# Kernel tuning notes

Hardware: AMD Instinct MI355X
Metric: run time of the kernel (lower is better)

The kernel has to match this reference:

```python
import jax, jax.numpy as jnp
import numpy as np

B, S, H = 32, 256, 256
D = 2 * H          # BiLSTM output dim (hidden_dim*2)
F = 1024           # total fragment count across the batch
T = 5              # tagset size


def setup_inputs() -> dict:
    key = jax.random.key(0)
    ks = jax.random.split(key, 9)
    en_output = jax.random.normal(ks[0], (B, S, D), jnp.float32)
    # descending lengths, first sentence defines seq_length = S
    lengths = jnp.sort(jax.random.randint(ks[1], (B,), S // 2, S + 1))[::-1]
    lengths = lengths.at[0].set(S)
    frag_b = jax.random.randint(ks[2], (F,), 0, B)
    frag_s = jax.random.randint(ks[3], (F,), 0, S // 2 - 8)
    width = jax.random.randint(ks[4], (F,), 1, 8)
    frag_e = frag_s + width  # end exclusive, always <= lengths[frag_b]
    att_w = jax.random.normal(ks[5], (3 * D, D), jnp.float32) / np.float32(np.sqrt(3 * D))
    att_b = jax.random.normal(ks[6], (3 * D,), jnp.float32) * 0.01
    tag_w = jax.random.normal(ks[7], (T, 4 * D), jnp.float32) / np.float32(np.sqrt(4 * D))
    tag_b = jax.random.normal(ks[8], (T,), jnp.float32) * 0.01
    return {"en_output": en_output, "lengths": lengths, "frag_b": frag_b,
            "frag_s": frag_s, "frag_e": frag_e, "att_w": att_w, "att_b": att_b,
            "tag_w": tag_w, "tag_b": tag_b}


def reference(en_output, lengths, frag_b, frag_s, frag_e, att_w, att_b, tag_w, tag_b):
    Fn = frag_b.shape[0]
    Bn, Sn, Dn = en_output.shape
    dtype = en_output.dtype
    pos = jnp.arange(Sn)                                            # [S]
    in_span = (pos[None, :] >= frag_s[:, None]) & (pos[None, :] < frag_e[:, None])  # [F,S]
    memory = en_output[frag_b]                                      # [F,S,D] gather per fragment
    # word_state = sum of hidden states over the span (segment-sum via mask)
    word_state = jnp.einsum('fs,fsd->fd', in_span.astype(dtype), memory)
    l_word = en_output[frag_b, frag_s]                              # [F,D]
    r_word = en_output[frag_b, frag_e - 1]                          # [F,D]
    span = jnp.concatenate([l_word, word_state, r_word], axis=-1)   # [F,3D]
    # attention mask: the span itself and all padding positions are masked out
    att_mask = in_span | (pos[None, :] >= lengths[frag_b][:, None])  # [F,S]
    seq_len = lengths[0]
    # position distance (int), then position weight 1 - dist/seq_len
    pos_dis = jnp.where(pos[None, :] < frag_s[:, None], frag_s[:, None] - pos[None, :],
                jnp.where(pos[None, :] >= frag_e[:, None], pos[None, :] - frag_e[:, None] + 1,
                          seq_len)).astype(dtype)
    pos_weight = 1.0 - pos_dis / seq_len.astype(dtype)
    final = pos_weight[:, :, None] * memory                         # [F,S,D]
    # att(final) @ span == final @ (att_w.T span) + att_b.span ; att_w is [3D, D] (torch Linear weight)
    v = span @ att_w                                                # [F,D]
    c = span @ att_b                                                # [F]
    scores = jnp.tanh(jnp.einsum('fsd,fd->fs', final, v) + c[:, None])
    scores = jnp.where(att_mask, jnp.asarray(-1e4, dtype), scores)
    att = jax.nn.softmax(scores, axis=1)                            # [F,S]
    mix = jnp.einsum('fs,fsd->fd', att, final)                      # [F,D]
    mix_state = jnp.concatenate([span, mix], axis=-1)               # [F,4D]
    logits = mix_state @ tag_w.T + tag_b                            # [F,T]
    return jax.nn.log_softmax(logits, axis=1)
```

## Files before the change

### kernel.cpp

```cpp
#include <hip/hip_runtime.h>
#include <math.h>

#define BB 32
#define SS 256
#define DD 512
#define FF 1024
#define TT 5
#define K3 1536
#define K4 2048
#define GK 1536
#define SK 4
#define KCH (GK / SK)

__device__ __forceinline__ float wave_reduce_sum(float x) {
#pragma unroll
  for (int o = 32; o > 0; o >>= 1) x += __shfl_xor(x, o);
  return x;
}

__device__ __forceinline__ float row16_sum(float x) {
  int y;
  y = __builtin_amdgcn_mov_dpp(__float_as_int(x), 0x121, 0xf, 0xf, true);
  x += __int_as_float(y);
  y = __builtin_amdgcn_mov_dpp(__float_as_int(x), 0x122, 0xf, 0xf, true);
  x += __int_as_float(y);
  y = __builtin_amdgcn_mov_dpp(__float_as_int(x), 0x124, 0xf, 0xf, true);
  x += __int_as_float(y);
  y = __builtin_amdgcn_mov_dpp(__float_as_int(x), 0x128, 0xf, 0xf, true);
  x += __int_as_float(y);
  return x;
}

__device__ __forceinline__ float fast_tanh(float x) {
  float ax = fabsf(x);
  float t = __expf(-2.f * ax);
  float r = (1.f - t) / (1.f + t);
  return x < 0.f ? -r : r;
}

__global__ __launch_bounds__(1024)
void bucket_kernel(const int* __restrict__ fb, int* __restrict__ order) {
  __shared__ int cnt[BB];
  __shared__ int start[BB];
  int t = threadIdx.x;
  if (t < BB) cnt[t] = 0;
  __syncthreads();
  int b = fb[t];
  int r = atomicAdd(&cnt[b], 1);
  __syncthreads();
  if (t == 0) {
    int pos = 0;
    for (int x = 0; x < 8; ++x) {
      int sb[4] = {x, 15 - x, 16 + x, 31 - x};
      for (int j = 0; j < 4; ++j) { start[sb[j]] = pos; pos += cnt[sb[j]]; }
    }
  }
  __syncthreads();
  order[start[b] + r] = t;
}

__global__ __launch_bounds__(128)
void span_kernel(const float* __restrict__ en, const int* __restrict__ fb,
                 const int* __restrict__ fs, const int* __restrict__ fe,
                 const float* __restrict__ att_b, const int* __restrict__ order,
                 float* __restrict__ span, float* __restrict__ cvec)
{
  int bid = blockIdx.x;
  int f = order[(bid & 7) * (FF / 8) + (bid >> 3)];
  int t = threadIdx.x;
  int b = fb[f], s = fs[f], e = fe[f];
  const float* base = en + (size_t)b * SS * DD;
  int d0 = t * 4;
  float4 lw = *(const float4*)(base + (size_t)s * DD + d0);
  float4 rw = *(const float4*)(base + (size_t)(e - 1) * DD + d0);
  float4 wsum = make_float4(0.f, 0.f, 0.f, 0.f);
  for (int p = s; p < e; ++p) {
    float4 m = *(const float4*)(base + (size_t)p * DD + d0);
    wsum.x += m.x; wsum.y += m.y; wsum.z += m.z; wsum.w += m.w;
  }
  float* sp = span + (size_t)f * K3;
  *(float4*)(sp + d0) = lw;
  *(float4*)(sp + DD + d0) = wsum;
  *(float4*)(sp + 2 * DD + d0) = rw;
  float4 a0 = *(const float4*)(att_b + d0);
  float4 a1 = *(const float4*)(att_b + DD + d0);
  float4 a2 = *(const float4*)(att_b + 2 * DD + d0);
  float part = lw.x*a0.x + lw.y*a0.y + lw.z*a0.z + lw.w*a0.w
             + wsum.x*a1.x + wsum.y*a1.y + wsum.z*a1.z + wsum.w*a1.w
             + rw.x*a2.x + rw.y*a2.y + rw.z*a2.z + rw.w*a2.w;
  part = wave_reduce_sum(part);
  __shared__ float red[2];
  if ((t & 63) == 0) red[t >> 6] = part;
  __syncthreads();
  if (t == 0) cvec[f] = red[0] + red[1];
}

__global__ __launch_bounds__(256)
void gemm_v(const float* __restrict__ A,
            const float* __restrict__ Bw,
            float* __restrict__ Cpart)
{
  const int BM = 64, BN = 64, BK = 16;
  const int NIT = KCH / BK;
  __shared__ float As[BK][BM + 4];
  __shared__ float Bs[BK][BN + 4];
  int t = threadIdx.x;
  int n0 = blockIdx.x * BN;
  int m0 = blockIdx.y * BM;
  int kbase = blockIdx.z * KCH;

  int ar = t >> 2;
  int ac = (t & 3) * 4;
  int br = t >> 4;
  int bc = (t & 15) * 4;
  int tm = (t >> 4) * 4;
  int tn = (t & 15) * 4;

  float acc[4][4] = {};

  const float* Aptr = A  + (size_t)(m0 + ar) * GK + kbase + ac;
  const float* Bptr = Bw + (size_t)(kbase + br) * DD + n0 + bc;

  float4 av = *(const float4*)(Aptr);
  float4 bv = *(const float4*)(Bptr);

  for (int it = 0; it < NIT; ++it) {
    __syncthreads();
    As[ac + 0][ar] = av.x;
    As[ac + 1][ar] = av.y;
    As[ac + 2][ar] = av.z;
    As[ac + 3][ar] = av.w;
    *(float4*)(&Bs[br][bc]) = bv;
    __syncthreads();
    if (it + 1 < NIT) {
      av = *(const float4*)(Aptr + (it + 1) * BK);
      bv = *(const float4*)(Bptr + (size_t)(it + 1) * BK * DD);
    }
#pragma unroll
    for (int k = 0; k < BK; ++k) {
      float4 a = *(float4*)(&As[k][tm]);
      float4 b = *(float4*)(&Bs[k][tn]);
      acc[0][0] += a.x * b.x; acc[0][1] += a.x * b.y; acc[0][2] += a.x * b.z; acc[0][3] += a.x * b.w;
      acc[1][0] += a.y * b.x; acc[1][1] += a.y * b.y; acc[1][2] += a.y * b.z; acc[1][3] += a.y * b.w;
      acc[2][0] += a.z * b.x; acc[2][1] += a.z * b.y; acc[2][2] += a.z * b.z; acc[2][3] += a.z * b.w;
      acc[3][0] += a.w * b.x; acc[3][1] += a.w * b.y; acc[3][2] += a.w * b.z; acc[3][3] += a.w * b.w;
    }
  }
  float* Cp = Cpart + (size_t)blockIdx.z * FF * DD;
#pragma unroll
  for (int i = 0; i < 4; ++i) {
    *(float4*)(Cp + (size_t)(m0 + tm + i) * DD + n0 + tn) =
        make_float4(acc[i][0], acc[i][1], acc[i][2], acc[i][3]);
  }
}

__global__ __launch_bounds__(256, 4)
void frag_kernel(const float* __restrict__ en, const int* __restrict__ lengths,
                 const int* __restrict__ fb, const int* __restrict__ fs,
                 const int* __restrict__ fe,
                 const float* __restrict__ span, const float* __restrict__ cvec,
                 const float* __restrict__ vpart,
                 const float* __restrict__ tag_w, const float* __restrict__ tag_b,
                 const int* __restrict__ order,
                 float* __restrict__ out)
{
  __shared__ float v_lds[DD];
  __shared__ float buf[4][DD];
  __shared__ float wsum[4];
  __shared__ float mix_lds[DD];
  __shared__ float pl[4 * TT];
  __shared__ float l5[TT];

  int bid = blockIdx.x;
  int f = order[(bid & 7) * (FF / 8) + (bid >> 3)];
  int t = threadIdx.x;
  int lane = t & 63, wv = t >> 6;
  int b = fb[f], s = fs[f], e = fe[f];
  int lenb = lengths[b];
  float seqlen = (float)lengths[0];
  float invseq = 1.f / seqlen;
  float c = cvec[f];
  const float* mem = en + (size_t)b * SS * DD;

  if (t < 128) {
    float4 v0 = *(const float4*)(vpart + (size_t)f * DD + t * 4);
    float4 v1 = *(const float4*)(vpart + (size_t)FF * DD + (size_t)f * DD + t * 4);
    float4 v2 = *(const float4*)(vpart + 2 * (size_t)FF * DD + (size_t)f * DD + t * 4);
    float4 v3 = *(const float4*)(vpart + 3 * (size_t)FF * DD + (size_t)f * DD + t * 4);
    *(float4*)(v_lds + t * 4) = make_float4(v0.x + v1.x + v2.x + v3.x,
                                            v0.y + v1.y + v2.y + v3.y,
                                            v0.z + v1.z + v2.z + v3.z,
                                            v0.w + v1.w + v2.w + v3.w);
  }
  __syncthreads();

  float4 va = *(float4*)(v_lds + lane * 8);
  float4 vb = *(float4*)(v_lds + lane * 8 + 4);
  float ssum = 0.f;
  float am[8] = {0.f, 0.f, 0.f, 0.f, 0.f, 0.f, 0.f, 0.f};

  int rows = lenb - wv * 64;
  if (rows > 64) rows = 64;
  for (int i0 = 0; i0 < rows; i0 += 8) {
    float4 R0[8], R1[8];
    float d8[8];
#pragma unroll
    for (int k = 0; k < 8; ++k) {
      if (i0 + k < rows) {
        int p = wv * 64 + i0 + k;
        const float* row = mem + (size_t)p * DD + lane * 8;
        R0[k] = *(const float4*)(row);
        R1[k] = *(const float4*)(row + 4);
        d8[k] = R0[k].x*va.x + R0[k].y*va.y + R0[k].z*va.z + R0[k].w*va.w
              + R1[k].x*vb.x + R1[k].y*vb.y + R1[k].z*vb.z + R1[k].w*vb.w;
      } else {
        d8[k] = 0.f;
      }
    }
#pragma unroll
    for (int k = 0; k < 8; ++k) d8[k] = row16_sum(d8[k]);
#pragma unroll
    for (int k = 0; k < 8; ++k) d8[k] += __shfl_xor(d8[k], 16);
#pragma unroll
    for (int k = 0; k < 8; ++k) d8[k] += __shfl_xor(d8[k], 32);
#pragma unroll
    for (int k = 0; k < 8; ++k) {
      int p = wv * 64 + i0 + k;
      bool live = (i0 + k < rows) && !(p >= s && p < e);
      if (live) {
        float dis = (p < s) ? (float)(s - p) : (float)(p - e + 1);
        float pw = 1.f - dis * invseq;
        float sc = fast_tanh(pw * d8[k] + c);
        float u = __expf(sc - 1.f);
        ssum += u;
        float upw = u * pw;
        am[0] += upw * R0[k].x; am[1] += upw * R0[k].y; am[2] += upw * R0[k].z; am[3] += upw * R0[k].w;
        am[4] += upw * R1[k].x; am[5] += upw * R1[k].y; am[6] += upw * R1[k].z; am[7] += upw * R1[k].w;
      }
    }
  }
  if (lane == 0) wsum[wv] = ssum;
  *(float4*)(&buf[wv][lane * 8])     = make_float4(am[0], am[1], am[2], am[3]);
  *(float4*)(&buf[wv][lane * 8 + 4]) = make_float4(am[4], am[5], am[6], am[7]);
  __syncthreads();
  {
    float S = wsum[0] + wsum[1] + wsum[2] + wsum[3];
    float inv = 1.f / S;
    int d0 = t * 2;
    mix_lds[d0]     = (buf[0][d0] + buf[1][d0] + buf[2][d0] + buf[3][d0]) * inv;
    mix_lds[d0 + 1] = (buf[0][d0 + 1] + buf[1][d0 + 1] + buf[2][d0 + 1] + buf[3][d0 + 1]) * inv;
  }
  __syncthreads();

  float vals[8];
  int idx = t * 8;
  if (idx < K3) {
    const float* sp = span + (size_t)f * K3 + idx;
    float4 x0 = *(const float4*)(sp);
    float4 x1 = *(const float4*)(sp + 4);
    vals[0]=x0.x; vals[1]=x0.y; vals[2]=x0.z; vals[3]=x0.w;
    vals[4]=x1.x; vals[5]=x1.y; vals[6]=x1.z; vals[7]=x1.w;
  } else {
#pragma unroll
    for (int j = 0; j < 8; ++j) vals[j] = mix_lds[idx - K3 + j];
  }
  float acc5[TT];
#pragma unroll
  for (int tg = 0; tg < TT; ++tg) {
    const float* twr = tag_w + (size_t)tg * K4 + idx;
    float a = 0.f;
#pragma unroll
    for (int j = 0; j < 8; ++j) a += vals[j] * twr[j];
    acc5[tg] = wave_reduce_sum(a);
  }
  if (lane == 0) {
#pragma unroll
    for (int tg = 0; tg < TT; ++tg) pl[wv * TT + tg] = acc5[tg];
  }
  __syncthreads();
  if (t < TT) {
    l5[t] = pl[t] + pl[TT + t] + pl[2 * TT + t] + pl[3 * TT + t] + tag_b[t];
  }
  __syncthreads();
  if (t == 0) {
    float mm = l5[0];
#pragma unroll
    for (int j = 1; j < TT; ++j) mm = fmaxf(mm, l5[j]);
    float se = 0.f;
#pragma unroll
    for (int j = 0; j < TT; ++j) se += __expf(l5[j] - mm);
    float lse = mm + logf(se);
#pragma unroll
    for (int j = 0; j < TT; ++j) out[(size_t)f * TT + j] = l5[j] - lse;
  }
}

extern "C" void kernel_launch(void* const* d_in, const int* in_sizes, int n_in,
                              void* d_out, int out_size, void* d_ws, size_t ws_size,
                              hipStream_t stream) {
  const float* en      = (const float*)d_in[0];
  const int*   lengths = (const int*)d_in[1];
  const int*   frag_b  = (const int*)d_in[2];
  const int*   frag_s  = (const int*)d_in[3];
  const int*   frag_e  = (const int*)d_in[4];
  const float* att_w   = (const float*)d_in[5];
  const float* att_b   = (const float*)d_in[6];
  const float* tag_w   = (const float*)d_in[7];
  const float* tag_b   = (const float*)d_in[8];
  float* out = (float*)d_out;

  float* span  = (float*)d_ws;
  float* cvec  = span + (size_t)FF * K3;
  float* vpart = cvec + FF;
  int*   order = (int*)(vpart + (size_t)SK * FF * DD);

  bucket_kernel<<<1, FF, 0, stream>>>(frag_b, order);
  span_kernel<<<FF, 128, 0, stream>>>(en, frag_b, frag_s, frag_e, att_b, order, span, cvec);
  gemm_v<<<dim3(8, 16, SK), 256, 0, stream>>>(span, att_w, vpart);
  frag_kernel<<<FF, 256, 0, stream>>>(en, lengths, frag_b, frag_s, frag_e,
                                      span, cvec, vpart, tag_w, tag_b, order, out);
}
```

Baseline: 146.0 us.

## Split each wave into four 16-lane groups processing separate rows

Restructures the attention scan so each wave processes four sequence rows at once, each handled by a 16-lane group covering the full 512-wide row. This removes the cross-row shuffle reductions (xor 16/32) per row, leaving only a DPP row16 reduction. In exchange, per-thread accumulators grow to 32 floats plus 32 staged values, and the partial-sum LDS buffer grows fourfold to 16 partials, raising register and LDS pressure.

Result: faster. 130.9 us (-10.3%).

```diff
diff --git a/kernel.cpp b/kernel.cpp
--- a/kernel.cpp
+++ b/kernel.cpp
@@ -165,8 +165,8 @@
                  float* __restrict__ out)
 {
   __shared__ float v_lds[DD];
-  __shared__ float buf[4][DD];
-  __shared__ float wsum[4];
+  __shared__ float buf[16][DD];
+  __shared__ float wsum[16];
   __shared__ float mix_lds[DD];
   __shared__ float pl[4 * TT];
   __shared__ float l5[TT];
@@ -175,6 +175,8 @@
   int f = order[(bid & 7) * (FF / 8) + (bid >> 3)];
   int t = threadIdx.x;
   int lane = t & 63, wv = t >> 6;
+  int g = lane >> 4;
+  int j = lane & 15;
   int b = fb[f], s = fs[f], e = fe[f];
   int lenb = lengths[b];
   float seqlen = (float)lengths[0];
@@ -194,61 +196,65 @@
   }
   __syncthreads();
 
-  float4 va = *(float4*)(v_lds + lane * 8);
-  float4 vb = *(float4*)(v_lds + lane * 8 + 4);
+  float4 vr[8];
+#pragma unroll
+  for (int q = 0; q < 8; ++q) vr[q] = *(float4*)(v_lds + q * 64 + j * 4);
+
+  float4 am8[8];
+#pragma unroll
+  for (int q = 0; q < 8; ++q) am8[q] = make_float4(0.f, 0.f, 0.f, 0.f);
   float ssum = 0.f;
-  float am[8] = {0.f, 0.f, 0.f, 0.f, 0.f, 0.f, 0.f, 0.f};
 
   int rows = lenb - wv * 64;
   if (rows > 64) rows = 64;
-  for (int i0 = 0; i0 < rows; i0 += 8) {
-    float4 R0[8], R1[8];
-    float d8[8];
-#pragma unroll
-    for (int k = 0; k < 8; ++k) {
-      if (i0 + k < rows) {
-        int p = wv * 64 + i0 + k;
-        const float* row = mem + (size_t)p * DD + lane * 8;
-        R0[k] = *(const float4*)(row);
-        R1[k] = *(const float4*)(row + 4);
-        d8[k] = R0[k].x*va.x + R0[k].y*va.y + R0[k].z*va.z + R0[k].w*va.w
-              + R1[k].x*vb.x + R1[k].y*vb.y + R1[k].z*vb.z + R1[k].w*vb.w;
-      } else {
-        d8[k] = 0.f;
-      }
-    }
-#pragma unroll
-    for (int k = 0; k < 8; ++k) d8[k] = row16_sum(d8[k]);
-#pragma unroll
-    for (int k = 0; k < 8; ++k) d8[k] += __shfl_xor(d8[k], 16);
-#pragma unroll
-    for (int k = 0; k < 8; ++k) d8[k] += __shfl_xor(d8[k], 32);
-#pragma unroll
-    for (int k = 0; k < 8; ++k) {
-      int p = wv * 64 + i0 + k;
-      bool live = (i0 + k < rows) && !(p >= s && p < e);
-      if (live) {
-        float dis = (p < s) ? (float)(s - p) : (float)(p - e + 1);
-        float pw = 1.f - dis * invseq;
-        float sc = fast_tanh(pw * d8[k] + c);
-        float u = __expf(sc - 1.f);
-        ssum += u;
-        float upw = u * pw;
-        am[0] += upw * R0[k].x; am[1] += upw * R0[k].y; am[2] += upw * R0[k].z; am[3] += upw * R0[k].w;
-        am[4] += upw * R1[k].x; am[5] += upw * R1[k].y; am[6] += upw * R1[k].z; am[7] += upw * R1[k].w;
-      }
-    }
-  }
-  if (lane == 0) wsum[wv] = ssum;
-  *(float4*)(&buf[wv][lane * 8])     = make_float4(am[0], am[1], am[2], am[3]);
-  *(float4*)(&buf[wv][lane * 8 + 4]) = make_float4(am[4], am[5], am[6], am[7]);
-  __syncthreads();
+  if (rows < 0) rows = 0;
+
+  for (int i0 = 0; i0 < rows; i0 += 4) {
+    int r = wv * 64 + i0 + g;
+    const float* row = mem + (size_t)r * DD;
+    float4 st[8];
+    float part = 0.f;
+#pragma unroll
+    for (int q = 0; q < 8; ++q) {
+      st[q] = *(const float4*)(row + q * 64 + j * 4);
+      part += st[q].x * vr[q].x + st[q].y * vr[q].y
+            + st[q].z * vr[q].z + st[q].w * vr[q].w;
+    }
+    float d = row16_sum(part);
+    bool live = (i0 + g < rows) && !(r >= s && r < e);
+    float dis = (r < s) ? (float)(s - r) : (float)(r - e + 1);
+    float pw = 1.f - dis * invseq;
+    float sc = fast_tanh(pw * d + c);
+    float u = live ? __expf(sc - 1.f) : 0.f;
+    ssum += u;
+    float upw = u * pw;
+#pragma unroll
+    for (int q = 0; q < 8; ++q) {
+      am8[q].x += upw * st[q].x;
+      am8[q].y += upw * st[q].y;
+      am8[q].z += upw * st[q].z;
+      am8[q].w += upw * st[q].w;
+    }
+  }
+
+  int part_id = wv * 4 + g;
+  if (j == 0) wsum[part_id] = ssum;
+#pragma unroll
+  for (int q = 0; q < 8; ++q)
+    *(float4*)(&buf[part_id][q * 64 + j * 4]) = am8[q];
+  __syncthreads();
+
   {
-    float S = wsum[0] + wsum[1] + wsum[2] + wsum[3];
+    float S = 0.f;
+#pragma unroll
+    for (int i = 0; i < 16; ++i) S += wsum[i];
     float inv = 1.f / S;
     int d0 = t * 2;
-    mix_lds[d0]     = (buf[0][d0] + buf[1][d0] + buf[2][d0] + buf[3][d0]) * inv;
-    mix_lds[d0 + 1] = (buf[0][d0 + 1] + buf[1][d0 + 1] + buf[2][d0 + 1] + buf[3][d0 + 1]) * inv;
+    float a0 = 0.f, a1 = 0.f;
+#pragma unroll
+    for (int i = 0; i < 16; ++i) { a0 += buf[i][d0]; a1 += buf[i][d0 + 1]; }
+    mix_lds[d0]     = a0 * inv;
+    mix_lds[d0 + 1] = a1 * inv;
   }
   __syncthreads();
 
@@ -262,7 +268,7 @@
     vals[4]=x1.x; vals[5]=x1.y; vals[6]=x1.z; vals[7]=x1.w;
   } else {
 #pragma unroll
-    for (int j = 0; j < 8; ++j) vals[j] = mix_lds[idx - K3 + j];
+    for (int jj = 0; jj < 8; ++jj) vals[jj] = mix_lds[idx - K3 + jj];
   }
   float acc5[TT];
 #pragma unroll
@@ -270,7 +276,7 @@
     const float* twr = tag_w + (size_t)tg * K4 + idx;
     float a = 0.f;
 #pragma unroll
-    for (int j = 0; j < 8; ++j) a += vals[j] * twr[j];
+    for (int jj = 0; jj < 8; ++jj) a += vals[jj] * twr[jj];
     acc5[tg] = wave_reduce_sum(a);
   }
   if (lane == 0) {
@@ -285,13 +291,13 @@
   if (t == 0) {
     float mm = l5[0];
 #pragma unroll
-    for (int j = 1; j < TT; ++j) mm = fmaxf(mm, l5[j]);
+    for (int jj = 1; jj < TT; ++jj) mm = fmaxf(mm, l5[jj]);
     float se = 0.f;
 #pragma unroll
-    for (int j = 0; j < TT; ++j) se += __expf(l5[j] - mm);
+    for (int jj = 0; jj < TT; ++jj) se += __expf(l5[jj] - mm);
     float lse = mm + logf(se);
 #pragma unroll
-    for (int j = 0; j < TT; ++j) out[(size_t)f * TT + j] = l5[j] - lse;
+    for (int jj = 0; jj < TT; ++jj) out[(size_t)f * TT + jj] = l5[jj] - lse;
   }
 }
 
```
